# Performance work log

Measured on AMD Instinct MI355X. Metric: run time of the kernel, lower is better.

Reference implementation:

```python
import jax, jax.numpy as jnp
import numpy as np
from jax import lax

B, T, IN, HID, RANK, OUT = 256, 1024, 3, 512, 4, 3


def setup_inputs() -> dict:
    key = jax.random.key(0)
    ks = jax.random.split(key, 7)
    return {
        "x": jax.random.normal(ks[0], (B, T, IN), dtype=jnp.float32),
        "hidden": jnp.zeros((B, HID), dtype=jnp.float32),  # None in torch == zero recurrence
        "U": jax.random.normal(ks[1], (RANK, HID), dtype=jnp.float32) * 0.06,
        "V": jax.random.normal(ks[2], (RANK, HID), dtype=jnp.float32) * 0.06,
        "W_in": jax.random.normal(ks[3], (HID, IN), dtype=jnp.float32) * 0.1,
        "b_in": jax.random.normal(ks[4], (HID,), dtype=jnp.float32) * 0.1,
        "W_out": jax.random.normal(ks[5], (OUT, HID), dtype=jnp.float32) * 0.1,
        "b_out": jax.random.normal(ks[6], (OUT,), dtype=jnp.float32) * 0.1,
    }


def reference(x, hidden, U, V, W_in, b_in, W_out, b_out):
    # Precompute input projection for all timesteps (same math as per-step Linear)
    input_w = jnp.einsum('bti,hi->bth', x, W_in) + b_in  # [B,T,HID]

    def step(h, iw_t):
        # hidden @ V.T @ U : low-rank recurrence through rank-r bottleneck
        h_new = jnp.tanh((h @ V.T) @ U + iw_t)  # [B,HID]
        return h_new, h_new

    h_last, r = lax.scan(step, hidden, input_w.transpose(1, 0, 2))  # r: [T,B,HID]
    r_out = r.transpose(1, 0, 2)  # [B,T,HID]
    output = jnp.einsum('bth,oh->bto', r_out, W_out) + b_out  # [B,T,OUT]
    return output, h_last, r_out
```

## Files before the change

kernel.cpp:

```cpp
#include <hip/hip_runtime.h>

#define NB 256
#define NT 1024
#define NH 512
#define NI 3
#define NO 3

template<int CTRL>
__device__ __forceinline__ float dpp_add(float x) {
  int y = __builtin_amdgcn_update_dpp(0, __float_as_int(x), CTRL, 0xf, 0xf, false);
  return x + __int_as_float(y);
}

__device__ __forceinline__ float wave_sum63(float x) {
  x = dpp_add<0x111>(x);
  x = dpp_add<0x112>(x);
  x = dpp_add<0x114>(x);
  x = dpp_add<0x118>(x);
  x = dpp_add<0x142>(x);
  x = dpp_add<0x143>(x);
  return x;
}

__device__ __forceinline__ float bcast_lane63(float x) {
  return __int_as_float(__builtin_amdgcn_readlane(__float_as_int(x), 63));
}

__device__ __forceinline__ float fast_tanh(float x) {
  float e = __builtin_amdgcn_exp2f(x * 2.885390081777927f);
  float r = __builtin_amdgcn_rcpf(e + 1.0f);
  return fmaf(-2.0f, r, 1.0f);
}

__global__ __launch_bounds__(64, 1)
void lowrank_rnn_kernel(const float* __restrict__ x,
                        const float* __restrict__ hidden,
                        const float* __restrict__ U,
                        const float* __restrict__ V,
                        const float* __restrict__ W_in,
                        const float* __restrict__ b_in,
                        const float* __restrict__ W_out,
                        const float* __restrict__ b_out,
                        float* __restrict__ out_y,
                        float* __restrict__ out_h,
                        float* __restrict__ out_r) {
  const int b = blockIdx.x;
  const int lane = threadIdx.x;

  __shared__ float xs[NT * NI];

  {
    const float4* src = (const float4*)(x + (size_t)b * NT * NI);
    float4* dst = (float4*)xs;
#pragma unroll
    for (int i = 0; i < (NT * NI / 4) / 64; ++i)
      dst[i * 64 + lane] = src[i * 64 + lane];
  }

  float Uv[4][8], Vv[4][8];
#pragma unroll
  for (int r = 0; r < 4; ++r) {
    float4 u0 = ((const float4*)U)[r * 128 + lane];
    float4 u1 = ((const float4*)U)[r * 128 + 64 + lane];
    Uv[r][0] = u0.x; Uv[r][1] = u0.y; Uv[r][2] = u0.z; Uv[r][3] = u0.w;
    Uv[r][4] = u1.x; Uv[r][5] = u1.y; Uv[r][6] = u1.z; Uv[r][7] = u1.w;
    float4 v0 = ((const float4*)V)[r * 128 + lane];
    float4 v1 = ((const float4*)V)[r * 128 + 64 + lane];
    Vv[r][0] = v0.x; Vv[r][1] = v0.y; Vv[r][2] = v0.z; Vv[r][3] = v0.w;
    Vv[r][4] = v1.x; Vv[r][5] = v1.y; Vv[r][6] = v1.z; Vv[r][7] = v1.w;
  }

  float Wi[8][3];
#pragma unroll
  for (int j = 0; j < 8; ++j) {
    int h = (j < 4) ? (4 * lane + j) : (256 + 4 * lane + (j - 4));
    Wi[j][0] = W_in[h * 3 + 0];
    Wi[j][1] = W_in[h * 3 + 1];
    Wi[j][2] = W_in[h * 3 + 2];
  }

  float bin[8];
  {
    float4 b0 = ((const float4*)b_in)[lane];
    float4 b1 = ((const float4*)b_in)[64 + lane];
    bin[0] = b0.x; bin[1] = b0.y; bin[2] = b0.z; bin[3] = b0.w;
    bin[4] = b1.x; bin[5] = b1.y; bin[6] = b1.z; bin[7] = b1.w;
  }

  float Wo[3][8];
#pragma unroll
  for (int o = 0; o < 3; ++o) {
    float4 w0 = ((const float4*)W_out)[o * 128 + lane];
    float4 w1 = ((const float4*)W_out)[o * 128 + 64 + lane];
    Wo[o][0] = w0.x; Wo[o][1] = w0.y; Wo[o][2] = w0.z; Wo[o][3] = w0.w;
    Wo[o][4] = w1.x; Wo[o][5] = w1.y; Wo[o][6] = w1.z; Wo[o][7] = w1.w;
  }
  const float bo0 = b_out[0], bo1 = b_out[1], bo2 = b_out[2];

  float hv[8];
  {
    const float4* h4 = (const float4*)(hidden + (size_t)b * NH);
    float4 h0 = h4[lane];
    float4 h1 = h4[64 + lane];
    hv[0] = h0.x; hv[1] = h0.y; hv[2] = h0.z; hv[3] = h0.w;
    hv[4] = h1.x; hv[5] = h1.y; hv[6] = h1.z; hv[7] = h1.w;
  }
  float p0, p1, p2, p3;
  {
    float s0 = 0.f, s1 = 0.f, s2 = 0.f, s3 = 0.f;
#pragma unroll
    for (int j = 0; j < 8; ++j) {
      s0 = fmaf(hv[j], Vv[0][j], s0);
      s1 = fmaf(hv[j], Vv[1][j], s1);
      s2 = fmaf(hv[j], Vv[2][j], s2);
      s3 = fmaf(hv[j], Vv[3][j], s3);
    }
    p0 = bcast_lane63(wave_sum63(s0));
    p1 = bcast_lane63(wave_sum63(s1));
    p2 = bcast_lane63(wave_sum63(s2));
    p3 = bcast_lane63(wave_sum63(s3));
  }

  __syncthreads();

  float cx0 = xs[0], cx1 = xs[1], cx2 = xs[2];

  float* rbase = out_r + (size_t)b * NT * NH;
  float* ybase = out_y + (size_t)b * NT * NO;

  for (int t = 0; t < NT; ++t) {
    float a[8];
#pragma unroll
    for (int j = 0; j < 8; ++j) {
      float v = bin[j];
      v = fmaf(cx0, Wi[j][0], v);
      v = fmaf(cx1, Wi[j][1], v);
      v = fmaf(cx2, Wi[j][2], v);
      v = fmaf(p0, Uv[0][j], v);
      v = fmaf(p1, Uv[1][j], v);
      v = fmaf(p2, Uv[2][j], v);
      v = fmaf(p3, Uv[3][j], v);
      a[j] = v;
    }
    if (t + 1 < NT) {
      cx0 = xs[(t + 1) * 3 + 0];
      cx1 = xs[(t + 1) * 3 + 1];
      cx2 = xs[(t + 1) * 3 + 2];
    }

#pragma unroll
    for (int j = 0; j < 8; ++j) hv[j] = fast_tanh(a[j]);

    float4* rp = (float4*)(rbase + (size_t)t * NH);
    rp[lane] = make_float4(hv[0], hv[1], hv[2], hv[3]);
    rp[64 + lane] = make_float4(hv[4], hv[5], hv[6], hv[7]);

    float s0 = 0.f, s1 = 0.f, s2 = 0.f, s3 = 0.f;
    float q0 = 0.f, q1 = 0.f, q2 = 0.f;
#pragma unroll
    for (int j = 0; j < 8; ++j) {
      s0 = fmaf(hv[j], Vv[0][j], s0);
      s1 = fmaf(hv[j], Vv[1][j], s1);
      s2 = fmaf(hv[j], Vv[2][j], s2);
      s3 = fmaf(hv[j], Vv[3][j], s3);
      q0 = fmaf(hv[j], Wo[0][j], q0);
      q1 = fmaf(hv[j], Wo[1][j], q1);
      q2 = fmaf(hv[j], Wo[2][j], q2);
    }
    s0 = wave_sum63(s0);
    s1 = wave_sum63(s1);
    s2 = wave_sum63(s2);
    s3 = wave_sum63(s3);
    q0 = wave_sum63(q0);
    q1 = wave_sum63(q1);
    q2 = wave_sum63(q2);
    p0 = bcast_lane63(s0);
    p1 = bcast_lane63(s1);
    p2 = bcast_lane63(s2);
    p3 = bcast_lane63(s3);
    if (lane == 63) {
      float* yp = ybase + t * NO;
      yp[0] = q0 + bo0;
      yp[1] = q1 + bo1;
      yp[2] = q2 + bo2;
    }
  }

  float4* hp = (float4*)(out_h + (size_t)b * NH);
  hp[lane] = make_float4(hv[0], hv[1], hv[2], hv[3]);
  hp[64 + lane] = make_float4(hv[4], hv[5], hv[6], hv[7]);
}

extern "C" void kernel_launch(void* const* d_in, const int* in_sizes, int n_in,
                              void* d_out, int out_size, void* d_ws, size_t ws_size,
                              hipStream_t stream) {
  const float* x      = (const float*)d_in[0];
  const float* hidden = (const float*)d_in[1];
  const float* U      = (const float*)d_in[2];
  const float* V      = (const float*)d_in[3];
  const float* W_in   = (const float*)d_in[4];
  const float* b_in   = (const float*)d_in[5];
  const float* W_out  = (const float*)d_in[6];
  const float* b_out  = (const float*)d_in[7];

  float* out = (float*)d_out;
  float* out_y = out;
  float* out_h = out + (size_t)NB * NT * NO;
  float* out_r = out_h + (size_t)NB * NH;

  hipLaunchKernelGGL(lowrank_rnn_kernel, dim3(NB), dim3(64), 0, stream,
                     x, hidden, U, V, W_in, b_in, W_out, b_out,
                     out_y, out_h, out_r);
}
```

Before: 892.4 us.

## Split recurrence across two waves and offload output writes to consumer waves

Uses four waves per batch row. Two waves split the hidden dimension to run the serial recurrence, combining rank-4 partial sums through shared memory each step, and log the projection vector per timestep. The other two waves lag by two steps, recompute the hidden state from the logged vector, write r and compute y, taking stores and output reductions off the critical chain. The trade-off is a block-wide barrier every timestep plus duplicated tanh/FMA work.

```diff
diff --git a/kernel.cpp b/kernel.cpp
--- a/kernel.cpp
+++ b/kernel.cpp
@@ -22,17 +22,13 @@
   return x;
 }
 
-__device__ __forceinline__ float bcast_lane63(float x) {
-  return __int_as_float(__builtin_amdgcn_readlane(__float_as_int(x), 63));
-}
-
 __device__ __forceinline__ float fast_tanh(float x) {
   float e = __builtin_amdgcn_exp2f(x * 2.885390081777927f);
   float r = __builtin_amdgcn_rcpf(e + 1.0f);
   return fmaf(-2.0f, r, 1.0f);
 }
 
-__global__ __launch_bounds__(64, 1)
+__global__ __launch_bounds__(256, 1)
 void lowrank_rnn_kernel(const float* __restrict__ x,
                         const float* __restrict__ hidden,
                         const float* __restrict__ U,
@@ -45,150 +41,200 @@
                         float* __restrict__ out_h,
                         float* __restrict__ out_r) {
   const int b = blockIdx.x;
-  const int lane = threadIdx.x;
+  const int tid = threadIdx.x;
+  const int lane = tid & 63;
+  const int wid = tid >> 6;
 
   __shared__ float xs[NT * NI];
+  __shared__ float4 p_used[NT + 1];
+  __shared__ float4 exch[2][2];
 
   {
     const float4* src = (const float4*)(x + (size_t)b * NT * NI);
     float4* dst = (float4*)xs;
 #pragma unroll
-    for (int i = 0; i < (NT * NI / 4) / 64; ++i)
-      dst[i * 64 + lane] = src[i * 64 + lane];
+    for (int i = 0; i < (NT * NI / 4) / 256; ++i)
+      dst[i * 256 + tid] = src[i * 256 + tid];
   }
-
-  float Uv[4][8], Vv[4][8];
-#pragma unroll
-  for (int r = 0; r < 4; ++r) {
-    float4 u0 = ((const float4*)U)[r * 128 + lane];
-    float4 u1 = ((const float4*)U)[r * 128 + 64 + lane];
-    Uv[r][0] = u0.x; Uv[r][1] = u0.y; Uv[r][2] = u0.z; Uv[r][3] = u0.w;
-    Uv[r][4] = u1.x; Uv[r][5] = u1.y; Uv[r][6] = u1.z; Uv[r][7] = u1.w;
-    float4 v0 = ((const float4*)V)[r * 128 + lane];
-    float4 v1 = ((const float4*)V)[r * 128 + 64 + lane];
-    Vv[r][0] = v0.x; Vv[r][1] = v0.y; Vv[r][2] = v0.z; Vv[r][3] = v0.w;
-    Vv[r][4] = v1.x; Vv[r][5] = v1.y; Vv[r][6] = v1.z; Vv[r][7] = v1.w;
+  __syncthreads();
+
+  if (wid < 2) {
+    float Uv[4][4], Vv[4][4];
+#pragma unroll
+    for (int r = 0; r < 4; ++r) {
+      float4 u = ((const float4*)U)[r * 128 + wid * 64 + lane];
+      Uv[r][0] = u.x; Uv[r][1] = u.y; Uv[r][2] = u.z; Uv[r][3] = u.w;
+      float4 v = ((const float4*)V)[r * 128 + wid * 64 + lane];
+      Vv[r][0] = v.x; Vv[r][1] = v.y; Vv[r][2] = v.z; Vv[r][3] = v.w;
+    }
+    float Wi[4][3];
+#pragma unroll
+    for (int j = 0; j < 4; ++j) {
+      int h = wid * 256 + 4 * lane + j;
+      Wi[j][0] = W_in[h * 3 + 0];
+      Wi[j][1] = W_in[h * 3 + 1];
+      Wi[j][2] = W_in[h * 3 + 2];
+    }
+    float bin[4];
+    {
+      float4 bb = ((const float4*)b_in)[wid * 64 + lane];
+      bin[0] = bb.x; bin[1] = bb.y; bin[2] = bb.z; bin[3] = bb.w;
+    }
+    float hv[4];
+    {
+      float4 h4 = ((const float4*)(hidden + (size_t)b * NH))[wid * 64 + lane];
+      hv[0] = h4.x; hv[1] = h4.y; hv[2] = h4.z; hv[3] = h4.w;
+    }
+
+    {
+      float s0 = 0.f, s1 = 0.f, s2 = 0.f, s3 = 0.f;
+#pragma unroll
+      for (int j = 0; j < 4; ++j) {
+        s0 = fmaf(hv[j], Vv[0][j], s0);
+        s1 = fmaf(hv[j], Vv[1][j], s1);
+        s2 = fmaf(hv[j], Vv[2][j], s2);
+        s3 = fmaf(hv[j], Vv[3][j], s3);
+      }
+      s0 = wave_sum63(s0); s1 = wave_sum63(s1);
+      s2 = wave_sum63(s2); s3 = wave_sum63(s3);
+      if (lane == 63) exch[1][wid] = make_float4(s0, s1, s2, s3);
+    }
+    __syncthreads();
+    float p0, p1, p2, p3;
+    {
+      float4 A = exch[1][0], Bv = exch[1][1];
+      p0 = A.x + Bv.x; p1 = A.y + Bv.y; p2 = A.z + Bv.z; p3 = A.w + Bv.w;
+      if (tid == 0) p_used[0] = make_float4(p0, p1, p2, p3);
+    }
+
+    float cx0 = xs[0], cx1 = xs[1], cx2 = xs[2];
+
+    for (int t = 0; t < NT + 2; ++t) {
+      if (t < NT) {
+        float a[4];
+#pragma unroll
+        for (int j = 0; j < 4; ++j) {
+          float v = bin[j];
+          v = fmaf(cx0, Wi[j][0], v);
+          v = fmaf(cx1, Wi[j][1], v);
+          v = fmaf(cx2, Wi[j][2], v);
+          v = fmaf(p0, Uv[0][j], v);
+          v = fmaf(p1, Uv[1][j], v);
+          v = fmaf(p2, Uv[2][j], v);
+          v = fmaf(p3, Uv[3][j], v);
+          a[j] = v;
+        }
+        if (t + 1 < NT) {
+          cx0 = xs[(t + 1) * 3 + 0];
+          cx1 = xs[(t + 1) * 3 + 1];
+          cx2 = xs[(t + 1) * 3 + 2];
+        }
+#pragma unroll
+        for (int j = 0; j < 4; ++j) hv[j] = fast_tanh(a[j]);
+
+        float s0 = 0.f, s1 = 0.f, s2 = 0.f, s3 = 0.f;
+#pragma unroll
+        for (int j = 0; j < 4; ++j) {
+          s0 = fmaf(hv[j], Vv[0][j], s0);
+          s1 = fmaf(hv[j], Vv[1][j], s1);
+          s2 = fmaf(hv[j], Vv[2][j], s2);
+          s3 = fmaf(hv[j], Vv[3][j], s3);
+        }
+        s0 = wave_sum63(s0); s1 = wave_sum63(s1);
+        s2 = wave_sum63(s2); s3 = wave_sum63(s3);
+        if (lane == 63) exch[t & 1][wid] = make_float4(s0, s1, s2, s3);
+      }
+      __syncthreads();
+      if (t < NT) {
+        float4 A = exch[t & 1][0], Bv = exch[t & 1][1];
+        p0 = A.x + Bv.x; p1 = A.y + Bv.y; p2 = A.z + Bv.z; p3 = A.w + Bv.w;
+        if (tid == 0) p_used[t + 1] = make_float4(p0, p1, p2, p3);
+      }
+    }
+
+    float4* hp = (float4*)(out_h + (size_t)b * NH);
+    hp[wid * 64 + lane] = make_float4(hv[0], hv[1], hv[2], hv[3]);
+  } else {
+    float Uv[4][8];
+#pragma unroll
+    for (int r = 0; r < 4; ++r) {
+      float4 u0 = ((const float4*)U)[r * 128 + lane];
+      float4 u1 = ((const float4*)U)[r * 128 + 64 + lane];
+      Uv[r][0] = u0.x; Uv[r][1] = u0.y; Uv[r][2] = u0.z; Uv[r][3] = u0.w;
+      Uv[r][4] = u1.x; Uv[r][5] = u1.y; Uv[r][6] = u1.z; Uv[r][7] = u1.w;
+    }
+    float Wi[8][3];
+#pragma unroll
+    for (int j = 0; j < 8; ++j) {
+      int h = (j < 4) ? (4 * lane + j) : (256 + 4 * lane + (j - 4));
+      Wi[j][0] = W_in[h * 3 + 0];
+      Wi[j][1] = W_in[h * 3 + 1];
+      Wi[j][2] = W_in[h * 3 + 2];
+    }
+    float bin[8];
+    {
+      float4 b0 = ((const float4*)b_in)[lane];
+      float4 b1 = ((const float4*)b_in)[64 + lane];
+      bin[0] = b0.x; bin[1] = b0.y; bin[2] = b0.z; bin[3] = b0.w;
+      bin[4] = b1.x; bin[5] = b1.y; bin[6] = b1.z; bin[7] = b1.w;
+    }
+    float Wo[3][8];
+#pragma unroll
+    for (int o = 0; o < 3; ++o) {
+      float4 w0 = ((const float4*)W_out)[o * 128 + lane];
+      float4 w1 = ((const float4*)W_out)[o * 128 + 64 + lane];
+      Wo[o][0] = w0.x; Wo[o][1] = w0.y; Wo[o][2] = w0.z; Wo[o][3] = w0.w;
+      Wo[o][4] = w1.x; Wo[o][5] = w1.y; Wo[o][6] = w1.z; Wo[o][7] = w1.w;
+    }
+    const float bo0 = b_out[0], bo1 = b_out[1], bo2 = b_out[2];
+
+    __syncthreads();
+
+    float* rbase = out_r + (size_t)b * NT * NH;
+    float* ybase = out_y + (size_t)b * NT * NO;
+
+    for (int t = 0; t < NT + 2; ++t) {
+      const int tp = t - 2;
+      if (tp >= 0 && (tp & 1) == (wid & 1)) {
+        float4 pu = p_used[tp];
+        float cx0 = xs[tp * 3 + 0], cx1 = xs[tp * 3 + 1], cx2 = xs[tp * 3 + 2];
+        float hvv[8];
+#pragma unroll
+        for (int j = 0; j < 8; ++j) {
+          float v = bin[j];
+          v = fmaf(cx0, Wi[j][0], v);
+          v = fmaf(cx1, Wi[j][1], v);
+          v = fmaf(cx2, Wi[j][2], v);
+          v = fmaf(pu.x, Uv[0][j], v);
+          v = fmaf(pu.y, Uv[1][j], v);
+          v = fmaf(pu.z, Uv[2][j], v);
+          v = fmaf(pu.w, Uv[3][j], v);
+          hvv[j] = fast_tanh(v);
+        }
+        float4* rp = (float4*)(rbase + (size_t)tp * NH);
+        rp[lane] = make_float4(hvv[0], hvv[1], hvv[2], hvv[3]);
+        rp[64 + lane] = make_float4(hvv[4], hvv[5], hvv[6], hvv[7]);
+
+        float q0 = 0.f, q1 = 0.f, q2 = 0.f;
+#pragma unroll
+        for (int j = 0; j < 8; ++j) {
+          q0 = fmaf(hvv[j], Wo[0][j], q0);
+          q1 = fmaf(hvv[j], Wo[1][j], q1);
+          q2 = fmaf(hvv[j], Wo[2][j], q2);
+        }
+        q0 = wave_sum63(q0);
+        q1 = wave_sum63(q1);
+        q2 = wave_sum63(q2);
+        if (lane == 63) {
+          float* yp = ybase + tp * NO;
+          yp[0] = q0 + bo0;
+          yp[1] = q1 + bo1;
+          yp[2] = q2 + bo2;
+        }
+      }
+      __syncthreads();
+    }
   }
-
-  float Wi[8][3];
-#pragma unroll
-  for (int j = 0; j < 8; ++j) {
-    int h = (j < 4) ? (4 * lane + j) : (256 + 4 * lane + (j - 4));
-    Wi[j][0] = W_in[h * 3 + 0];
-    Wi[j][1] = W_in[h * 3 + 1];
-    Wi[j][2] = W_in[h * 3 + 2];
-  }
-
-  float bin[8];
-  {
-    float4 b0 = ((const float4*)b_in)[lane];
-    float4 b1 = ((const float4*)b_in)[64 + lane];
-    bin[0] = b0.x; bin[1] = b0.y; bin[2] = b0.z; bin[3] = b0.w;
-    bin[4] = b1.x; bin[5] = b1.y; bin[6] = b1.z; bin[7] = b1.w;
-  }
-
-  float Wo[3][8];
-#pragma unroll
-  for (int o = 0; o < 3; ++o) {
-    float4 w0 = ((const float4*)W_out)[o * 128 + lane];
-    float4 w1 = ((const float4*)W_out)[o * 128 + 64 + lane];
-    Wo[o][0] = w0.x; Wo[o][1] = w0.y; Wo[o][2] = w0.z; Wo[o][3] = w0.w;
-    Wo[o][4] = w1.x; Wo[o][5] = w1.y; Wo[o][6] = w1.z; Wo[o][7] = w1.w;
-  }
-  const float bo0 = b_out[0], bo1 = b_out[1], bo2 = b_out[2];
-
-  float hv[8];
-  {
-    const float4* h4 = (const float4*)(hidden + (size_t)b * NH);
-    float4 h0 = h4[lane];
-    float4 h1 = h4[64 + lane];
-    hv[0] = h0.x; hv[1] = h0.y; hv[2] = h0.z; hv[3] = h0.w;
-    hv[4] = h1.x; hv[5] = h1.y; hv[6] = h1.z; hv[7] = h1.w;
-  }
-  float p0, p1, p2, p3;
-  {
-    float s0 = 0.f, s1 = 0.f, s2 = 0.f, s3 = 0.f;
-#pragma unroll
-    for (int j = 0; j < 8; ++j) {
-      s0 = fmaf(hv[j], Vv[0][j], s0);
-      s1 = fmaf(hv[j], Vv[1][j], s1);
-      s2 = fmaf(hv[j], Vv[2][j], s2);
-      s3 = fmaf(hv[j], Vv[3][j], s3);
-    }
-    p0 = bcast_lane63(wave_sum63(s0));
-    p1 = bcast_lane63(wave_sum63(s1));
-    p2 = bcast_lane63(wave_sum63(s2));
-    p3 = bcast_lane63(wave_sum63(s3));
-  }
-
-  __syncthreads();
-
-  float cx0 = xs[0], cx1 = xs[1], cx2 = xs[2];
-
-  float* rbase = out_r + (size_t)b * NT * NH;
-  float* ybase = out_y + (size_t)b * NT * NO;
-
-  for (int t = 0; t < NT; ++t) {
-    float a[8];
-#pragma unroll
-    for (int j = 0; j < 8; ++j) {
-      float v = bin[j];
-      v = fmaf(cx0, Wi[j][0], v);
-      v = fmaf(cx1, Wi[j][1], v);
-      v = fmaf(cx2, Wi[j][2], v);
-      v = fmaf(p0, Uv[0][j], v);
-      v = fmaf(p1, Uv[1][j], v);
-      v = fmaf(p2, Uv[2][j], v);
-      v = fmaf(p3, Uv[3][j], v);
-      a[j] = v;
-    }
-    if (t + 1 < NT) {
-      cx0 = xs[(t + 1) * 3 + 0];
-      cx1 = xs[(t + 1) * 3 + 1];
-      cx2 = xs[(t + 1) * 3 + 2];
-    }
-
-#pragma unroll
-    for (int j = 0; j < 8; ++j) hv[j] = fast_tanh(a[j]);
-
-    float4* rp = (float4*)(rbase + (size_t)t * NH);
-    rp[lane] = make_float4(hv[0], hv[1], hv[2], hv[3]);
-    rp[64 + lane] = make_float4(hv[4], hv[5], hv[6], hv[7]);
-
-    float s0 = 0.f, s1 = 0.f, s2 = 0.f, s3 = 0.f;
-    float q0 = 0.f, q1 = 0.f, q2 = 0.f;
-#pragma unroll
-    for (int j = 0; j < 8; ++j) {
-      s0 = fmaf(hv[j], Vv[0][j], s0);
-      s1 = fmaf(hv[j], Vv[1][j], s1);
-      s2 = fmaf(hv[j], Vv[2][j], s2);
-      s3 = fmaf(hv[j], Vv[3][j], s3);
-      q0 = fmaf(hv[j], Wo[0][j], q0);
-      q1 = fmaf(hv[j], Wo[1][j], q1);
-      q2 = fmaf(hv[j], Wo[2][j], q2);
-    }
-    s0 = wave_sum63(s0);
-    s1 = wave_sum63(s1);
-    s2 = wave_sum63(s2);
-    s3 = wave_sum63(s3);
-    q0 = wave_sum63(q0);
-    q1 = wave_sum63(q1);
-    q2 = wave_sum63(q2);
-    p0 = bcast_lane63(s0);
-    p1 = bcast_lane63(s1);
-    p2 = bcast_lane63(s2);
-    p3 = bcast_lane63(s3);
-    if (lane == 63) {
-      float* yp = ybase + t * NO;
-      yp[0] = q0 + bo0;
-      yp[1] = q1 + bo1;
-      yp[2] = q2 + bo2;
-    }
-  }
-
-  float4* hp = (float4*)(out_h + (size_t)b * NH);
-  hp[lane] = make_float4(hv[0], hv[1], hv[2], hv[3]);
-  hp[64 + lane] = make_float4(hv[4], hv[5], hv[6], hv[7]);
 }
 
 extern "C" void kernel_launch(void* const* d_in, const int* in_sizes, int n_in,
@@ -208,7 +254,7 @@
   float* out_h = out + (size_t)NB * NT * NO;
   float* out_r = out_h + (size_t)NB * NH;
 
-  hipLaunchKernelGGL(lowrank_rnn_kernel, dim3(NB), dim3(64), 0, stream,
+  hipLaunchKernelGGL(lowrank_rnn_kernel, dim3(NB), dim3(256), 0, stream,
                      x, hidden, U, V, W_in, b_in, W_out, b_out,
                      out_y, out_h, out_r);
 }
```

Result: faster. 844.6 us (-5.4%).

## Warp-specialize recurrence: producer, serial scan, and writer waves with double buffers

Applied to the files above, without the earlier changes.

The single wave per batch is split into four waves. Wave 1 precomputes the input projection for the next 16-step chunk into shared memory, wave 0 runs only the serial tanh/low-rank recurrence into a shared h buffer, and waves 2-3 write r to global memory and compute the output projection for the previous chunk. The goal is to take global stores and the output reductions off the latency-critical recurrence path and overlap them with the scan. In exchange it adds shared-memory traffic, a block barrier per chunk, and 128KB of LDS per block.

```diff
diff --git a/kernel.cpp b/kernel.cpp
--- a/kernel.cpp
+++ b/kernel.cpp
@@ -5,6 +5,8 @@
 #define NH 512
 #define NI 3
 #define NO 3
+#define CH 16
+#define NC (NT / CH)
 
 template<int CTRL>
 __device__ __forceinline__ float dpp_add(float x) {
@@ -32,7 +34,7 @@
   return fmaf(-2.0f, r, 1.0f);
 }
 
-__global__ __launch_bounds__(64, 1)
+__global__ __launch_bounds__(256, 1)
 void lowrank_rnn_kernel(const float* __restrict__ x,
                         const float* __restrict__ hidden,
                         const float* __restrict__ U,
@@ -45,68 +47,40 @@
                         float* __restrict__ out_h,
                         float* __restrict__ out_r) {
   const int b = blockIdx.x;
-  const int lane = threadIdx.x;
-
-  __shared__ float xs[NT * NI];
-
-  {
-    const float4* src = (const float4*)(x + (size_t)b * NT * NI);
-    float4* dst = (float4*)xs;
-#pragma unroll
-    for (int i = 0; i < (NT * NI / 4) / 64; ++i)
-      dst[i * 64 + lane] = src[i * 64 + lane];
-  }
+  const int tid = threadIdx.x;
+  const int lane = tid & 63;
+  const int wid = tid >> 6;
+
+  __shared__ float c_buf[2][CH][NH];
+  __shared__ float h_buf[2][CH][NH];
 
   float Uv[4][8], Vv[4][8];
-#pragma unroll
-  for (int r = 0; r < 4; ++r) {
-    float4 u0 = ((const float4*)U)[r * 128 + lane];
-    float4 u1 = ((const float4*)U)[r * 128 + 64 + lane];
-    Uv[r][0] = u0.x; Uv[r][1] = u0.y; Uv[r][2] = u0.z; Uv[r][3] = u0.w;
-    Uv[r][4] = u1.x; Uv[r][5] = u1.y; Uv[r][6] = u1.z; Uv[r][7] = u1.w;
-    float4 v0 = ((const float4*)V)[r * 128 + lane];
-    float4 v1 = ((const float4*)V)[r * 128 + 64 + lane];
-    Vv[r][0] = v0.x; Vv[r][1] = v0.y; Vv[r][2] = v0.z; Vv[r][3] = v0.w;
-    Vv[r][4] = v1.x; Vv[r][5] = v1.y; Vv[r][6] = v1.z; Vv[r][7] = v1.w;
-  }
-
-  float Wi[8][3];
-#pragma unroll
-  for (int j = 0; j < 8; ++j) {
-    int h = (j < 4) ? (4 * lane + j) : (256 + 4 * lane + (j - 4));
-    Wi[j][0] = W_in[h * 3 + 0];
-    Wi[j][1] = W_in[h * 3 + 1];
-    Wi[j][2] = W_in[h * 3 + 2];
-  }
-
-  float bin[8];
-  {
-    float4 b0 = ((const float4*)b_in)[lane];
-    float4 b1 = ((const float4*)b_in)[64 + lane];
-    bin[0] = b0.x; bin[1] = b0.y; bin[2] = b0.z; bin[3] = b0.w;
-    bin[4] = b1.x; bin[5] = b1.y; bin[6] = b1.z; bin[7] = b1.w;
-  }
-
+  float hv[8];
+  float p0 = 0.f, p1 = 0.f, p2 = 0.f, p3 = 0.f;
+  float Wi[8][3], bin[8];
   float Wo[3][8];
-#pragma unroll
-  for (int o = 0; o < 3; ++o) {
-    float4 w0 = ((const float4*)W_out)[o * 128 + lane];
-    float4 w1 = ((const float4*)W_out)[o * 128 + 64 + lane];
-    Wo[o][0] = w0.x; Wo[o][1] = w0.y; Wo[o][2] = w0.z; Wo[o][3] = w0.w;
-    Wo[o][4] = w1.x; Wo[o][5] = w1.y; Wo[o][6] = w1.z; Wo[o][7] = w1.w;
-  }
-  const float bo0 = b_out[0], bo1 = b_out[1], bo2 = b_out[2];
-
-  float hv[8];
-  {
-    const float4* h4 = (const float4*)(hidden + (size_t)b * NH);
-    float4 h0 = h4[lane];
-    float4 h1 = h4[64 + lane];
-    hv[0] = h0.x; hv[1] = h0.y; hv[2] = h0.z; hv[3] = h0.w;
-    hv[4] = h1.x; hv[5] = h1.y; hv[6] = h1.z; hv[7] = h1.w;
-  }
-  float p0, p1, p2, p3;
-  {
+  float bo0 = 0.f, bo1 = 0.f, bo2 = 0.f;
+
+
+  if (wid == 0) {
+#pragma unroll
+    for (int r = 0; r < 4; ++r) {
+      float4 u0 = ((const float4*)U)[r * 128 + lane];
+      float4 u1 = ((const float4*)U)[r * 128 + 64 + lane];
+      Uv[r][0] = u0.x; Uv[r][1] = u0.y; Uv[r][2] = u0.z; Uv[r][3] = u0.w;
+      Uv[r][4] = u1.x; Uv[r][5] = u1.y; Uv[r][6] = u1.z; Uv[r][7] = u1.w;
+      float4 v0 = ((const float4*)V)[r * 128 + lane];
+      float4 v1 = ((const float4*)V)[r * 128 + 64 + lane];
+      Vv[r][0] = v0.x; Vv[r][1] = v0.y; Vv[r][2] = v0.z; Vv[r][3] = v0.w;
+      Vv[r][4] = v1.x; Vv[r][5] = v1.y; Vv[r][6] = v1.z; Vv[r][7] = v1.w;
+    }
+    {
+      const float4* h4 = (const float4*)(hidden + (size_t)b * NH);
+      float4 h0 = h4[lane];
+      float4 h1 = h4[64 + lane];
+      hv[0] = h0.x; hv[1] = h0.y; hv[2] = h0.z; hv[3] = h0.w;
+      hv[4] = h1.x; hv[5] = h1.y; hv[6] = h1.z; hv[7] = h1.w;
+    }
     float s0 = 0.f, s1 = 0.f, s2 = 0.f, s3 = 0.f;
 #pragma unroll
     for (int j = 0; j < 8; ++j) {
@@ -119,76 +93,158 @@
     p1 = bcast_lane63(wave_sum63(s1));
     p2 = bcast_lane63(wave_sum63(s2));
     p3 = bcast_lane63(wave_sum63(s3));
+  } else if (wid == 1) {
+#pragma unroll
+    for (int j = 0; j < 8; ++j) {
+      int h = (j < 4) ? (4 * lane + j) : (256 + 4 * lane + (j - 4));
+      Wi[j][0] = W_in[h * 3 + 0];
+      Wi[j][1] = W_in[h * 3 + 1];
+      Wi[j][2] = W_in[h * 3 + 2];
+    }
+    {
+      float4 b0 = ((const float4*)b_in)[lane];
+      float4 b1 = ((const float4*)b_in)[64 + lane];
+      bin[0] = b0.x; bin[1] = b0.y; bin[2] = b0.z; bin[3] = b0.w;
+      bin[4] = b1.x; bin[5] = b1.y; bin[6] = b1.z; bin[7] = b1.w;
+    }
+    const float* xb = x + (size_t)b * NT * NI;
+    for (int s = 0; s < CH; ++s) {
+      const float* xp = xb + s * NI;
+      float x0 = xp[0], x1 = xp[1], x2 = xp[2];
+      float cv[8];
+#pragma unroll
+      for (int j = 0; j < 8; ++j) {
+        float v = bin[j];
+        v = fmaf(x0, Wi[j][0], v);
+        v = fmaf(x1, Wi[j][1], v);
+        v = fmaf(x2, Wi[j][2], v);
+        cv[j] = v;
+      }
+      *(float4*)&c_buf[0][s][4 * lane] = make_float4(cv[0], cv[1], cv[2], cv[3]);
+      *(float4*)&c_buf[0][s][256 + 4 * lane] = make_float4(cv[4], cv[5], cv[6], cv[7]);
+    }
+  } else {
+#pragma unroll
+    for (int o = 0; o < 3; ++o) {
+      float4 w0 = ((const float4*)W_out)[o * 128 + lane];
+      float4 w1 = ((const float4*)W_out)[o * 128 + 64 + lane];
+      Wo[o][0] = w0.x; Wo[o][1] = w0.y; Wo[o][2] = w0.z; Wo[o][3] = w0.w;
+      Wo[o][4] = w1.x; Wo[o][5] = w1.y; Wo[o][6] = w1.z; Wo[o][7] = w1.w;
+    }
+    bo0 = b_out[0]; bo1 = b_out[1]; bo2 = b_out[2];
   }
 
   __syncthreads();
-
-  float cx0 = xs[0], cx1 = xs[1], cx2 = xs[2];
 
   float* rbase = out_r + (size_t)b * NT * NH;
   float* ybase = out_y + (size_t)b * NT * NO;
 
-  for (int t = 0; t < NT; ++t) {
-    float a[8];
-#pragma unroll
-    for (int j = 0; j < 8; ++j) {
-      float v = bin[j];
-      v = fmaf(cx0, Wi[j][0], v);
-      v = fmaf(cx1, Wi[j][1], v);
-      v = fmaf(cx2, Wi[j][2], v);
-      v = fmaf(p0, Uv[0][j], v);
-      v = fmaf(p1, Uv[1][j], v);
-      v = fmaf(p2, Uv[2][j], v);
-      v = fmaf(p3, Uv[3][j], v);
-      a[j] = v;
-    }
-    if (t + 1 < NT) {
-      cx0 = xs[(t + 1) * 3 + 0];
-      cx1 = xs[(t + 1) * 3 + 1];
-      cx2 = xs[(t + 1) * 3 + 2];
-    }
-
-#pragma unroll
-    for (int j = 0; j < 8; ++j) hv[j] = fast_tanh(a[j]);
-
-    float4* rp = (float4*)(rbase + (size_t)t * NH);
-    rp[lane] = make_float4(hv[0], hv[1], hv[2], hv[3]);
-    rp[64 + lane] = make_float4(hv[4], hv[5], hv[6], hv[7]);
-
-    float s0 = 0.f, s1 = 0.f, s2 = 0.f, s3 = 0.f;
-    float q0 = 0.f, q1 = 0.f, q2 = 0.f;
-#pragma unroll
-    for (int j = 0; j < 8; ++j) {
-      s0 = fmaf(hv[j], Vv[0][j], s0);
-      s1 = fmaf(hv[j], Vv[1][j], s1);
-      s2 = fmaf(hv[j], Vv[2][j], s2);
-      s3 = fmaf(hv[j], Vv[3][j], s3);
-      q0 = fmaf(hv[j], Wo[0][j], q0);
-      q1 = fmaf(hv[j], Wo[1][j], q1);
-      q2 = fmaf(hv[j], Wo[2][j], q2);
-    }
-    s0 = wave_sum63(s0);
-    s1 = wave_sum63(s1);
-    s2 = wave_sum63(s2);
-    s3 = wave_sum63(s3);
-    q0 = wave_sum63(q0);
-    q1 = wave_sum63(q1);
-    q2 = wave_sum63(q2);
-    p0 = bcast_lane63(s0);
-    p1 = bcast_lane63(s1);
-    p2 = bcast_lane63(s2);
-    p3 = bcast_lane63(s3);
-    if (lane == 63) {
-      float* yp = ybase + t * NO;
-      yp[0] = q0 + bo0;
-      yp[1] = q1 + bo1;
-      yp[2] = q2 + bo2;
-    }
+  for (int k = 0; k <= NC; ++k) {
+    if (wid == 0) {
+      if (k < NC) {
+        const float (*cc)[NH] = c_buf[k & 1];
+        float (*hh)[NH] = h_buf[k & 1];
+        float4 ca = *(const float4*)&cc[0][4 * lane];
+        float4 cb = *(const float4*)&cc[0][256 + 4 * lane];
+#pragma unroll 4
+        for (int s = 0; s < CH; ++s) {
+          float a[8];
+          a[0] = fmaf(p3, Uv[3][0], fmaf(p2, Uv[2][0], fmaf(p1, Uv[1][0], fmaf(p0, Uv[0][0], ca.x))));
+          a[1] = fmaf(p3, Uv[3][1], fmaf(p2, Uv[2][1], fmaf(p1, Uv[1][1], fmaf(p0, Uv[0][1], ca.y))));
+          a[2] = fmaf(p3, Uv[3][2], fmaf(p2, Uv[2][2], fmaf(p1, Uv[1][2], fmaf(p0, Uv[0][2], ca.z))));
+          a[3] = fmaf(p3, Uv[3][3], fmaf(p2, Uv[2][3], fmaf(p1, Uv[1][3], fmaf(p0, Uv[0][3], ca.w))));
+          a[4] = fmaf(p3, Uv[3][4], fmaf(p2, Uv[2][4], fmaf(p1, Uv[1][4], fmaf(p0, Uv[0][4], cb.x))));
+          a[5] = fmaf(p3, Uv[3][5], fmaf(p2, Uv[2][5], fmaf(p1, Uv[1][5], fmaf(p0, Uv[0][5], cb.y))));
+          a[6] = fmaf(p3, Uv[3][6], fmaf(p2, Uv[2][6], fmaf(p1, Uv[1][6], fmaf(p0, Uv[0][6], cb.z))));
+          a[7] = fmaf(p3, Uv[3][7], fmaf(p2, Uv[2][7], fmaf(p1, Uv[1][7], fmaf(p0, Uv[0][7], cb.w))));
+          if (s + 1 < CH) {
+            ca = *(const float4*)&cc[s + 1][4 * lane];
+            cb = *(const float4*)&cc[s + 1][256 + 4 * lane];
+          }
+#pragma unroll
+          for (int j = 0; j < 8; ++j) hv[j] = fast_tanh(a[j]);
+          *(float4*)&hh[s][4 * lane] = make_float4(hv[0], hv[1], hv[2], hv[3]);
+          *(float4*)&hh[s][256 + 4 * lane] = make_float4(hv[4], hv[5], hv[6], hv[7]);
+          float s0 = 0.f, s1 = 0.f, s2 = 0.f, s3 = 0.f;
+#pragma unroll
+          for (int j = 0; j < 8; ++j) {
+            s0 = fmaf(hv[j], Vv[0][j], s0);
+            s1 = fmaf(hv[j], Vv[1][j], s1);
+            s2 = fmaf(hv[j], Vv[2][j], s2);
+            s3 = fmaf(hv[j], Vv[3][j], s3);
+          }
+          s0 = wave_sum63(s0);
+          s1 = wave_sum63(s1);
+          s2 = wave_sum63(s2);
+          s3 = wave_sum63(s3);
+          p0 = bcast_lane63(s0);
+          p1 = bcast_lane63(s1);
+          p2 = bcast_lane63(s2);
+          p3 = bcast_lane63(s3);
+        }
+      }
+    } else if (wid == 1) {
+      if (k + 1 < NC) {
+        const int tbase = (k + 1) * CH;
+        float (*cdst)[NH] = c_buf[(k + 1) & 1];
+        const float* xb = x + ((size_t)b * NT + tbase) * NI;
+        for (int s = 0; s < CH; ++s) {
+          const float* xp = xb + s * NI;
+          float x0 = xp[0], x1 = xp[1], x2 = xp[2];
+          float cv[8];
+#pragma unroll
+          for (int j = 0; j < 8; ++j) {
+            float v = bin[j];
+            v = fmaf(x0, Wi[j][0], v);
+            v = fmaf(x1, Wi[j][1], v);
+            v = fmaf(x2, Wi[j][2], v);
+            cv[j] = v;
+          }
+          *(float4*)&cdst[s][4 * lane] = make_float4(cv[0], cv[1], cv[2], cv[3]);
+          *(float4*)&cdst[s][256 + 4 * lane] = make_float4(cv[4], cv[5], cv[6], cv[7]);
+        }
+      }
+    } else {
+      if (k >= 1) {
+        const float (*hb)[NH] = h_buf[(k - 1) & 1];
+        const int tb = (k - 1) * CH;
+#pragma unroll 2
+        for (int si = 0; si < CH / 2; ++si) {
+          const int s = (wid - 2) * (CH / 2) + si;
+          const int t = tb + s;
+          float4 h0 = *(const float4*)&hb[s][4 * lane];
+          float4 h1 = *(const float4*)&hb[s][256 + 4 * lane];
+          float4* rp = (float4*)(rbase + (size_t)t * NH);
+          rp[lane] = h0;
+          rp[64 + lane] = h1;
+          float hvv[8] = {h0.x, h0.y, h0.z, h0.w, h1.x, h1.y, h1.z, h1.w};
+          float q0 = 0.f, q1 = 0.f, q2 = 0.f;
+#pragma unroll
+          for (int j = 0; j < 8; ++j) {
+            q0 = fmaf(hvv[j], Wo[0][j], q0);
+            q1 = fmaf(hvv[j], Wo[1][j], q1);
+            q2 = fmaf(hvv[j], Wo[2][j], q2);
+          }
+          q0 = wave_sum63(q0);
+          q1 = wave_sum63(q1);
+          q2 = wave_sum63(q2);
+          if (lane == 63) {
+            float* yp = ybase + t * NO;
+            yp[0] = q0 + bo0;
+            yp[1] = q1 + bo1;
+            yp[2] = q2 + bo2;
+          }
+        }
+      }
+    }
+    __syncthreads();
   }
 
-  float4* hp = (float4*)(out_h + (size_t)b * NH);
-  hp[lane] = make_float4(hv[0], hv[1], hv[2], hv[3]);
-  hp[64 + lane] = make_float4(hv[4], hv[5], hv[6], hv[7]);
+  if (wid == 0) {
+    float4* hp = (float4*)(out_h + (size_t)b * NH);
+    hp[lane] = make_float4(hv[0], hv[1], hv[2], hv[3]);
+    hp[64 + lane] = make_float4(hv[4], hv[5], hv[6], hv[7]);
+  }
 }
 
 extern "C" void kernel_launch(void* const* d_in, const int* in_sizes, int n_in,
@@ -208,7 +264,7 @@
   float* out_h = out + (size_t)NB * NT * NO;
   float* out_r = out_h + (size_t)NB * NH;
 
-  hipLaunchKernelGGL(lowrank_rnn_kernel, dim3(NB), dim3(64), 0, stream,
+  hipLaunchKernelGGL(lowrank_rnn_kernel, dim3(NB), dim3(256), 0, stream,
                      x, hidden, U, V, W_in, b_in, W_out, b_out,
                      out_y, out_h, out_r);
 }
```

Result: faster. 752.5 us (-15.7%).
